# Kernel optimization log

Hardware: AMD Instinct MI355X
Metric: run time of the kernel (lower is better)

The kernel has to match this reference:

```python
import jax, jax.numpy as jnp
import numpy as np

B, L, D = 1, 2048, 1024
H = 16
HD = D // H
BETA = 0.08
EPS = 1e-6


def setup_inputs() -> dict:
    key = jax.random.key(0)
    ks = jax.random.split(key, 12)
    sc = 1.0 / np.sqrt(D)
    inp = {
        'x': jax.random.normal(ks[0], (B, L, D), dtype=jnp.float32),
        'Wq': jax.random.normal(ks[1], (D, D), dtype=jnp.float32) * sc,
        'bq': jnp.zeros((D,), jnp.float32),
        'Wk': jax.random.normal(ks[2], (D, D), dtype=jnp.float32) * sc,
        'bk': jnp.zeros((D,), jnp.float32),
        'Wv': jax.random.normal(ks[3], (D, D), dtype=jnp.float32) * sc,
        'bv': jnp.zeros((D,), jnp.float32),
        'Wo': jax.random.normal(ks[4], (D, D), dtype=jnp.float32) * sc,
        'bo': jnp.zeros((D,), jnp.float32),
        'Wp': jax.random.normal(ks[5], (2 * H, D), dtype=jnp.float32) * sc,
        'bp': jnp.zeros((2 * H,), jnp.float32),
        'gamma': jnp.full((H,), -2.197224577, jnp.float32),
    }
    return inp


def _split(t):  # [B,L,D] -> [B,H,L,hd]
    return t.reshape(B, L, H, HD).transpose(0, 2, 1, 3)


def reference(x, Wq, bq, Wk, bk, Wv, bv, Wo, bo, Wp, bp, gamma):
    q = _split(x @ Wq.T + bq)
    k = _split(x @ Wk.T + bk)
    v = _split(x @ Wv.T + bv)

    # phase features: [B,L,2H] -> [B,H,L,2], L2-normalized (torch F.normalize: x / max(||x||, eps))
    ph = (x @ Wp.T + bp).reshape(B, L, H, 2).transpose(0, 2, 1, 3)
    nrm = jnp.maximum(jnp.linalg.norm(ph, axis=-1, keepdims=True), EPS)
    ph = ph / nrm
    c, s = ph[..., 0], ph[..., 1]  # [B,H,L]

    # rank-2 Gram interference bias: cos(dphi) = c_i c_j + s_i s_j -> [B,H,L,L]
    inter = c[..., :, None] * c[..., None, :] + s[..., :, None] * s[..., None, :]
    head_gate = jax.nn.sigmoid(gamma) * BETA  # active_heads_mask all ones (fraction=1.0)
    bias = inter * head_gate[None, :, None, None]

    scores = jnp.einsum('bhqd,bhkd->bhqk', q, k) / jnp.sqrt(jnp.float32(HD)) + bias
    attn = jax.nn.softmax(scores, axis=-1)
    out = jnp.einsum('bhqk,bhkd->bhqd', attn, v)
    out = out.transpose(0, 2, 1, 3).reshape(B, L, D)
    return out @ Wo.T + bo
```

## Files before the change

### kernel.cpp

```cpp
#include <hip/hip_runtime.h>
#include <stdint.h>

typedef unsigned short u16;
typedef unsigned int u32;

#define L_SEQ 2048
#define DMODEL 1024
#define NHEAD 16

using f32x4 = __attribute__((ext_vector_type(4))) float;
using f32x16 = __attribute__((ext_vector_type(16))) float;
using s16x8 = __attribute__((ext_vector_type(8))) short;
using s16x4 = __attribute__((ext_vector_type(4))) short;

__device__ __forceinline__ u16 f2b(float f) {
    union { float f; uint32_t u; } v; v.f = f;
    uint32_t r = v.u + 0x7fffu + ((v.u >> 16) & 1u);
    return (u16)(r >> 16);
}

__device__ __forceinline__ float b2f(u16 x) {
    union { uint32_t u; float f; } v; v.u = ((uint32_t)x) << 16;
    return v.f;
}

__device__ __forceinline__ u32 pk2(float a, float b) {
    return (u32)f2b(a) | ((u32)f2b(b) << 16);
}

__device__ __forceinline__ u32 cvtpk(float lo, float hi_) {
    u32 r;
    asm("v_cvt_pk_bf16_f32 %0, %1, %2" : "=v"(r) : "v"(lo), "v"(hi_));
    return r;
}

__device__ __forceinline__ void gld16(const void* g, void* l) {
    __builtin_amdgcn_global_load_lds(
        (__attribute__((address_space(1))) void*)(uintptr_t)g,
        (__attribute__((address_space(3))) void*)(uintptr_t)l,
        16, 0, 0);
}

__global__ __launch_bounds__(256)
void k_conv(const float* __restrict__ x, const float* __restrict__ wq,
            const float* __restrict__ wk, const float* __restrict__ wv,
            const float* __restrict__ wo, const float* __restrict__ wp,
            const float* __restrict__ bp,
            u16* __restrict__ xb, u16* __restrict__ wqb, u16* __restrict__ wkb,
            u16* __restrict__ wvb, u16* __restrict__ wob, u16* __restrict__ wpb,
            float* __restrict__ bpPad) {
    const int NX = L_SEQ * DMODEL / 8;
    const int NW = DMODEL * DMODEL / 8;
    const int NCONV = (NX + 4 * NW) / 256;
    const int NP = 32 * DMODEL / 8;
    const int bid = blockIdx.x, tid = threadIdx.x;

    if (bid < NCONV) {
        int i = bid * 256 + tid;
        const float* src; u16* dst; int j;
        if (i < NX) { src = x; dst = xb; j = i; }
        else {
            int t = i - NX; int sel = t >> 17; j = t & (NW - 1);
            src = (sel == 0) ? wq : (sel == 1) ? wk : (sel == 2) ? wv : wo;
            dst = (sel == 0) ? wqb : (sel == 1) ? wkb : (sel == 2) ? wvb : wob;
        }
        const float4* s4 = (const float4*)src;
        float4 a = s4[2 * j], b = s4[2 * j + 1];
        union { s16x8 v; u16 u[8]; } o;
        o.u[0] = f2b(a.x); o.u[1] = f2b(a.y); o.u[2] = f2b(a.z); o.u[3] = f2b(a.w);
        o.u[4] = f2b(b.x); o.u[5] = f2b(b.y); o.u[6] = f2b(b.z); o.u[7] = f2b(b.w);
        ((s16x8*)dst)[j] = o.v;
        return;
    }
    if (bid < NCONV + 32) {
        int i2 = (bid - NCONV) * 256 + tid;
        union { s16x8 v; u16 u[8]; } o;
        if (i2 < NP) {
            const float4* s4 = (const float4*)wp;
            float4 a = s4[2 * i2], b = s4[2 * i2 + 1];
            o.u[0] = f2b(a.x); o.u[1] = f2b(a.y); o.u[2] = f2b(a.z); o.u[3] = f2b(a.w);
            o.u[4] = f2b(b.x); o.u[5] = f2b(b.y); o.u[6] = f2b(b.z); o.u[7] = f2b(b.w);
        } else {
#pragma unroll
            for (int j = 0; j < 8; ++j) o.u[j] = 0;
        }
        ((s16x8*)wpb)[i2] = o.v;
        return;
    }
    if (tid < 64) bpPad[tid] = (tid < 32) ? bp[tid] : 0.f;
}

template <int MODE>
__global__ __launch_bounds__(256, 2)
void k_gemm64(const u16* __restrict__ A,
              const u16* __restrict__ B0, const u16* __restrict__ B1, const u16* __restrict__ B2,
              const u16* __restrict__ B3,
              const float* __restrict__ c0, const float* __restrict__ c1, const float* __restrict__ c2,
              const float* __restrict__ c3,
              void* __restrict__ Out, u16* __restrict__ Vt, float* __restrict__ Ph,
              int ldo, int K) {
    __shared__ u16 As[128 * 64];
    __shared__ u16 Bs[64 * 64];
    const int tid = threadIdx.x;
    const int w = tid >> 6, lane = tid & 63;
    const int wr = w >> 1, wc = w & 1;
    const int u = lane & 15, g = lane >> 4;
    const int lr = lane >> 3;
    const int cb = lane & 7;
    const int mt = blockIdx.x, nt = blockIdx.y;
    const int seg = nt >> 4, ntl = nt & 15;
    const u16* Bp = (seg == 0) ? B0 : (seg == 1) ? B1 : (seg == 2) ? B2 : B3;
    const float* biasp = (seg == 0) ? c0 : (seg == 1) ? c1 : (seg == 2) ? c2 : c3;

    const u16* Ab = A + (size_t)(mt * 128 + w * 32) * K;
    const u16* Bb = Bp + (size_t)(ntl * 64) * K;
    char* asB = (char*)As;
    char* bsB = (char*)Bs;

    f32x4 acc[4][2] = {};

    for (int k0 = 0; k0 < K; k0 += 64) {
#pragma unroll
        for (int c = 0; c < 4; ++c)
            gld16(Ab + (size_t)(c * 8 + lr) * K + k0 + ((cb ^ lr) * 8),
                  asB + (w * 32 + c * 8) * 128);
#pragma unroll
        for (int t = 0; t < 2; ++t)
            gld16(Bb + (size_t)(t * 32 + w * 8 + lr) * K + k0 + ((cb ^ lr) * 8),
                  bsB + t * 4096 + w * 1024);
        __syncthreads();
        const int x0 = (g * 16) ^ ((u & 7) << 4);
#pragma unroll
        for (int ks = 0; ks < 2; ++ks) {
            s16x8 af[4], bf[2];
#pragma unroll
            for (int i = 0; i < 4; ++i)
                af[i] = *(const s16x8*)(asB + (wr * 64 + i * 16 + u) * 128 + (x0 ^ (ks * 64)));
#pragma unroll
            for (int j = 0; j < 2; ++j)
                bf[j] = *(const s16x8*)(bsB + (wc * 32 + j * 16 + u) * 128 + (x0 ^ (ks * 64)));
#pragma unroll
            for (int i = 0; i < 4; ++i)
#pragma unroll
                for (int j = 0; j < 2; ++j)
                    acc[i][j] = __builtin_amdgcn_mfma_f32_16x16x32_bf16(af[i], bf[j], acc[i][j], 0, 0, 0);
        }
        __syncthreads();
    }

#pragma unroll
    for (int i = 0; i < 4; ++i) {
#pragma unroll
        for (int j = 0; j < 2; ++j) {
            const int row0 = mt * 128 + wr * 64 + i * 16 + g * 4;
            const int col = nt * 64 + wc * 32 + j * 16 + u;
            const int colseg = ntl * 64 + wc * 32 + j * 16 + u;
            const float bias = biasp[colseg];
            if (MODE == 0 && seg == 2) {
                union { s16x4 v; u16 us[4]; } p;
#pragma unroll
                for (int r = 0; r < 4; ++r) p.us[r] = f2b(acc[i][j][r] + bias);
                *(s16x4*)(Vt + (size_t)colseg * L_SEQ + row0) = p.v;
            } else if (MODE == 0 && seg == 3) {
#pragma unroll
                for (int r = 0; r < 4; ++r)
                    Ph[(size_t)(row0 + r) * 64 + colseg] = acc[i][j][r] + bias;
            } else {
#pragma unroll
                for (int r = 0; r < 4; ++r) {
                    float val = acc[i][j][r] + bias;
                    if (MODE == 1)
                        ((float*)Out)[(size_t)(row0 + r) * ldo + col] = val;
                    else
                        ((u16*)Out)[(size_t)(row0 + r) * ldo + col] = f2b(val);
                }
            }
        }
    }
}

__global__ __launch_bounds__(256)
void k_norm(const float* __restrict__ ph, float2* __restrict__ CSph) {
    int t = blockIdx.x * 256 + threadIdx.x;
    int m = t >> 4, h = t & 15;
    float c = ph[(size_t)m * 64 + 2 * h];
    float s = ph[(size_t)m * 64 + 2 * h + 1];
    float inv = 1.0f / fmaxf(sqrtf(c * c + s * s), 1e-6f);
    CSph[(size_t)h * L_SEQ + m] = make_float2(c * inv, s * inv);
}

__global__ __launch_bounds__(256, 2)
void k_attn(const u16* __restrict__ QKV, const u16* __restrict__ VtG,
            const float2* __restrict__ CSph,
            const float* __restrict__ gamma,
            u16* __restrict__ Op0, u16* __restrict__ Op1, u16* __restrict__ Op2,
            float2* __restrict__ ML) {
    const int h = blockIdx.y;
    const int s = blockIdx.z;
    const int qb = blockIdx.x * 128;
    const int tid = threadIdx.x;
    const int ww = tid >> 6, lane = tid & 63;
    const int q5 = lane & 31, hi = lane >> 5;
    const int ld = 3 * DMODEL;
    const int NT = (s == 2) ? 10 : 11;
    const int kbase = s * 11 * 64;
    const int BUF = 64 * 64 * 2;
    const float MFIX = 8.0f;

    __shared__ u16 Ks[2][64 * 64];
    __shared__ u16 Vs[2][64 * 64];

    const float LOG2E = 1.44269504088896f;
    const float sig = 1.0f / (1.0f + __expf(-gamma[h]));
    const float gateA = 0.64f * sig;
    const float SC2 = 0.125f * LOG2E;

    const u16* Qp = QKV + h * 64;
    const u16* Kp = QKV + DMODEL + h * 64 + (size_t)kbase * ld;
    const u16* VtH = VtG + (size_t)h * 64 * L_SEQ + kbase;
    const float2* CS = CSph + (size_t)h * L_SEQ;

    const int qrow = qb + ww * 32 + q5;
    s16x8 bq[4];
#pragma unroll
    for (int d = 0; d < 4; ++d)
        bq[d] = *(const s16x8*)(Qp + (size_t)qrow * ld + d * 16 + hi * 8);
    s16x8 bcs;
    {
        float2 cs = CS[qrow];
        union { u32 w[4]; s16x8 v; } t = {};
        t.w[0] = hi ? 0u : pk2(cs.x, cs.y);
        bcs = t.v;
    }

    unsigned dstOff[2]; size_t srcK[2], srcV[2];
#pragma unroll
    for (int t = 0; t < 2; ++t) {
        int ci = (ww * 2 + t) * 64 + lane;
        int row = ci >> 3, cb = ci & 7;
        dstOff[t] = (unsigned)((ww * 2 + t) * 1024);
        srcK[t] = (size_t)row * ld + (size_t)((cb ^ (row & 7)) * 8);
        srcV[t] = (size_t)row * L_SEQ + (size_t)((cb ^ (row & 7)) * 8);
    }
    char* ksBase = (char*)Ks;
    char* vsBase = (char*)Vs;
    const int swz = (q5 & 7) << 4;

#pragma unroll
    for (int t = 0; t < 2; ++t) {
        gld16(Kp + srcK[t], ksBase + dstOff[t]);
        gld16(VtH + srcV[t], vsBase + dstOff[t]);
    }
    __syncthreads();

    float lsum = 0.f;
    f32x16 oA = {}, oB = {};

    for (int kt = 0; kt < NT; ++kt) {
        const int cur = kt & 1;
        const char* kCur = ksBase + cur * BUF;
        const char* vCur = vsBase + cur * BUF;

        if (kt + 1 < NT) {
            const u16* Kn = Kp + (size_t)(kt + 1) * 64 * ld;
            const u16* Vn = VtH + (size_t)(kt + 1) * 64;
            char* kN = ksBase + (cur ^ 1) * BUF;
            char* vN = vsBase + (cur ^ 1) * BUF;
#pragma unroll
            for (int t = 0; t < 2; ++t) {
                gld16(Kn + srcK[t], kN + dstOff[t]);
                gld16(Vn + srcV[t], vN + dstOff[t]);
            }
        }

        s16x8 acs0, acs1;
        {
            float2 c0 = CS[kbase + kt * 64 + q5];
            float2 c1 = CS[kbase + kt * 64 + 32 + q5];
            union { u32 w[4]; s16x8 v; } t0 = {}, t1 = {};
            t0.w[0] = hi ? 0u : pk2(gateA * c0.x, gateA * c0.y);
            t1.w[0] = hi ? 0u : pk2(gateA * c1.x, gateA * c1.y);
            acs0 = t0.v; acs1 = t1.v;
        }

        f32x16 sf0 = {}, sf1 = {};
        __builtin_amdgcn_s_setprio(1);
#pragma unroll
        for (int d = 0; d < 4; ++d) {
            s16x8 ak0 = *(const s16x8*)(kCur + q5 * 128 + ((d * 32 + hi * 16) ^ swz));
            s16x8 ak1 = *(const s16x8*)(kCur + (32 + q5) * 128 + ((d * 32 + hi * 16) ^ swz));
            sf0 = __builtin_amdgcn_mfma_f32_32x32x16_bf16(ak0, bq[d], sf0, 0, 0, 0);
            sf1 = __builtin_amdgcn_mfma_f32_32x32x16_bf16(ak1, bq[d], sf1, 0, 0, 0);
        }
        sf0 = __builtin_amdgcn_mfma_f32_32x32x16_bf16(acs0, bcs, sf0, 0, 0, 0);
        sf1 = __builtin_amdgcn_mfma_f32_32x32x16_bf16(acs1, bcs, sf1, 0, 0, 0);
        __builtin_amdgcn_s_setprio(0);

#pragma unroll
        for (int r = 0; r < 16; ++r) sf0[r] = __builtin_amdgcn_exp2f(__builtin_fmaf(sf0[r], SC2, -MFIX));
#pragma unroll
        for (int r = 0; r < 16; ++r) sf1[r] = __builtin_amdgcn_exp2f(__builtin_fmaf(sf1[r], SC2, -MFIX));

#pragma unroll
        for (int r = 0; r < 16; ++r) lsum += sf0[r] + sf1[r];

        __builtin_amdgcn_s_setprio(1);
#define PV_SUBTILE(SFV, HALF, SU)                                                              \
        {                                                                                      \
            u32 Aw  = cvtpk(SFV[(HALF) * 8 + 0], SFV[(HALF) * 8 + 1]);                         \
            u32 A2w = cvtpk(SFV[(HALF) * 8 + 2], SFV[(HALF) * 8 + 3]);                         \
            u32 Bw  = cvtpk(SFV[(HALF) * 8 + 4], SFV[(HALF) * 8 + 5]);                         \
            u32 B2w = cvtpk(SFV[(HALF) * 8 + 6], SFV[(HALF) * 8 + 7]);                         \
            u32 xw  = (u32)__shfl_xor((int)(hi ? Aw : Bw), 32);                                \
            u32 x2w = (u32)__shfl_xor((int)(hi ? A2w : B2w), 32);                              \
            union { u32 w[4]; s16x8 v; } pa;                                                   \
            pa.w[0] = hi ? xw : Aw;   pa.w[1] = hi ? x2w : A2w;                                \
            pa.w[2] = hi ? Bw : xw;   pa.w[3] = hi ? B2w : x2w;                                \
            s16x8 bvA = *(const s16x8*)(vCur + q5 * 128 + (((SU) * 32 + hi * 16) ^ swz));      \
            s16x8 bvB = *(const s16x8*)(vCur + (32 + q5) * 128 + (((SU) * 32 + hi * 16) ^ swz));\
            oA = __builtin_amdgcn_mfma_f32_32x32x16_bf16(pa.v, bvA, oA, 0, 0, 0);              \
            oB = __builtin_amdgcn_mfma_f32_32x32x16_bf16(pa.v, bvB, oB, 0, 0, 0);              \
        }
        PV_SUBTILE(sf0, 0, 0)
        PV_SUBTILE(sf0, 1, 1)
        PV_SUBTILE(sf1, 0, 2)
        PV_SUBTILE(sf1, 1, 3)
#undef PV_SUBTILE
        __builtin_amdgcn_s_setprio(0);

        __syncthreads();
    }

    lsum += __shfl_xor(lsum, 32);

    u16* OpS = (s == 0) ? Op0 : (s == 1) ? Op1 : Op2;
    float2* MLS = ML + (size_t)(s * NHEAD + h) * L_SEQ;
#pragma unroll
    for (int r = 0; r < 16; ++r) {
        int q_r = qb + ww * 32 + (r & 3) + 8 * (r >> 2) + 4 * hi;
        OpS[(size_t)q_r * DMODEL + h * 64 + q5] = f2b(oA[r]);
        OpS[(size_t)q_r * DMODEL + h * 64 + 32 + q5] = f2b(oB[r]);
    }
    if (hi == 0)
        MLS[qb + ww * 32 + q5] = make_float2(MFIX, lsum);
}

__global__ __launch_bounds__(256)
void k_comb(const u16* __restrict__ Op0, const u16* __restrict__ Op1,
            const u16* __restrict__ Op2, const float2* __restrict__ ML,
            u16* __restrict__ attnb) {
    int t = blockIdx.x * 256 + threadIdx.x;
    int row = t >> 7, cg = t & 127;
    int col0 = cg * 8, h = cg >> 3;
    float2 ml0 = ML[(size_t)h * L_SEQ + row];
    float2 ml1 = ML[(size_t)(NHEAD + h) * L_SEQ + row];
    float2 ml2 = ML[(size_t)(2 * NHEAD + h) * L_SEQ + row];
    float M = fmaxf(fmaxf(ml0.x, ml1.x), ml2.x);
    float a0 = __builtin_amdgcn_exp2f(ml0.x - M);
    float a1 = __builtin_amdgcn_exp2f(ml1.x - M);
    float a2 = __builtin_amdgcn_exp2f(ml2.x - M);
    float inv = 1.0f / (ml0.y * a0 + ml1.y * a1 + ml2.y * a2);
    a0 *= inv; a1 *= inv; a2 *= inv;
    union { s16x8 v; u16 us[8]; } o0, o1, o2, wout;
    size_t off = (size_t)row * DMODEL + col0;
    o0.v = *(const s16x8*)(Op0 + off);
    o1.v = *(const s16x8*)(Op1 + off);
    o2.v = *(const s16x8*)(Op2 + off);
#pragma unroll
    for (int j = 0; j < 8; ++j)
        wout.us[j] = f2b(b2f(o0.us[j]) * a0 + b2f(o1.us[j]) * a1 + b2f(o2.us[j]) * a2);
    *(s16x8*)(attnb + off) = wout.v;
}

extern "C" void kernel_launch(void* const* d_in, const int* in_sizes, int n_in,
                              void* d_out, int out_size, void* d_ws, size_t ws_size,
                              hipStream_t stream) {
    const float* x  = (const float*)d_in[0];
    const float* Wq = (const float*)d_in[1];
    const float* bq = (const float*)d_in[2];
    const float* Wk = (const float*)d_in[3];
    const float* bk = (const float*)d_in[4];
    const float* Wv = (const float*)d_in[5];
    const float* bv = (const float*)d_in[6];
    const float* Wo = (const float*)d_in[7];
    const float* bo = (const float*)d_in[8];
    const float* Wp = (const float*)d_in[9];
    const float* bp = (const float*)d_in[10];
    const float* gamma = (const float*)d_in[11];
    float* out = (float*)d_out;

    char* ws = (char*)d_ws;
    u16* xb = (u16*)ws;   ws += (size_t)L_SEQ * DMODEL * 2;
    u16* wqb = (u16*)ws;  ws += (size_t)DMODEL * DMODEL * 2;
    u16* wkb = (u16*)ws;  ws += (size_t)DMODEL * DMODEL * 2;
    u16* wvb = (u16*)ws;  ws += (size_t)DMODEL * DMODEL * 2;
    u16* wob = (u16*)ws;  ws += (size_t)DMODEL * DMODEL * 2;
    u16* qkv = (u16*)ws;  ws += (size_t)L_SEQ * 3 * DMODEL * 2;
    u16* attnb = (u16*)ws; ws += (size_t)L_SEQ * DMODEL * 2;
    u16* VtG = (u16*)ws;  ws += (size_t)DMODEL * L_SEQ * 2;
    float2* CSph = (float2*)ws; ws += (size_t)NHEAD * L_SEQ * 8;
    u16* wpb = (u16*)ws;  ws += (size_t)64 * DMODEL * 2;
    float* bpPad = (float*)ws; ws += 64 * 4;
    float* phtmp = (float*)ws; ws += (size_t)L_SEQ * 64 * 4;

    u16* Op0 = xb;
    u16* Op1 = wqb;
    u16* Op2 = attnb;
    float2* ML = (float2*)wvb;

    k_conv<<<3072 + 32 + 1, 256, 0, stream>>>(x, Wq, Wk, Wv, Wo, Wp, bp,
                                              xb, wqb, wkb, wvb, wob, wpb, bpPad);

    k_gemm64<0><<<dim3(16, 49), 256, 0, stream>>>(xb, wqb, wkb, wvb, wpb,
                                                  bq, bk, bv, bpPad,
                                                  (void*)qkv, VtG, phtmp, 3 * DMODEL, DMODEL);

    k_norm<<<L_SEQ * NHEAD / 256, 256, 0, stream>>>(phtmp, CSph);

    k_attn<<<dim3(L_SEQ / 128, NHEAD, 3), 256, 0, stream>>>(qkv, VtG, CSph, gamma,
                                                            Op0, Op1, Op2, ML);

    k_comb<<<L_SEQ * DMODEL / 8 / 256, 256, 0, stream>>>(Op0, Op1, Op2, ML, attnb);

    k_gemm64<1><<<dim3(16, 16), 256, 0, stream>>>(attnb, wob, wob, wob, wob,
                                                  bo, bo, bo, bo,
                                                  (void*)out, nullptr, nullptr, DMODEL, DMODEL);
}
```

Measured before the change: 85.38 us.

## Triple-buffer K/V tiles with vmcnt waits and preload phase terms into LDS

Moves the attention K/V staging from double to triple buffering. Two tiles are now in flight, and each iteration waits on a partial vmcnt count plus a raw s_barrier instead of a full __syncthreads. The gated cos/sin phase terms for all key tiles are also computed once into LDS up front, so the loop no longer does global loads and packing for them. This hides more global-load latency, at the cost of extra LDS (about 50 KB per block), which may reduce occupancy under launch_bounds(256,2), and of fragile hand-counted vmcnt values.

```diff
diff --git a/kernel.cpp b/kernel.cpp
--- a/kernel.cpp
+++ b/kernel.cpp
@@ -207,8 +207,9 @@
     const int BUF = 64 * 64 * 2;
     const float MFIX = 8.0f;
 
-    __shared__ u16 Ks[2][64 * 64];
-    __shared__ u16 Vs[2][64 * 64];
+    __shared__ u16 Ks[3][64 * 64];
+    __shared__ u16 Vs[3][64 * 64];
+    __shared__ u32 csLDS[11 * 32 * 2];
 
     const float LOG2E = 1.44269504088896f;
     const float sig = 1.0f / (1.0f + __expf(-gamma[h]));
@@ -247,39 +248,48 @@
     const int swz = (q5 & 7) << 4;
 
 #pragma unroll
-    for (int t = 0; t < 2; ++t) {
-        gld16(Kp + srcK[t], ksBase + dstOff[t]);
-        gld16(VtH + srcV[t], vsBase + dstOff[t]);
+    for (int pt = 0; pt < 3; ++pt) {
+        if (pt < NT) {
+            const u16* Kn = Kp + (size_t)pt * 64 * ld;
+            const u16* Vn = VtH + (size_t)pt * 64;
+#pragma unroll
+            for (int t = 0; t < 2; ++t) {
+                gld16(Kn + srcK[t], ksBase + pt * BUF + dstOff[t]);
+                gld16(Vn + srcV[t], vsBase + pt * BUF + dstOff[t]);
+            }
+        }
+    }
+    for (int t = tid; t < NT * 32; t += 256) {
+        int kt = t >> 5, qq = t & 31;
+        float2 c0 = CS[kbase + kt * 64 + qq];
+        float2 c1 = CS[kbase + kt * 64 + 32 + qq];
+        csLDS[t * 2] = pk2(gateA * c0.x, gateA * c0.y);
+        csLDS[t * 2 + 1] = pk2(gateA * c1.x, gateA * c1.y);
     }
     __syncthreads();
 
     float lsum = 0.f;
     f32x16 oA = {}, oB = {};
+    int cur = 0;
 
     for (int kt = 0; kt < NT; ++kt) {
-        const int cur = kt & 1;
         const char* kCur = ksBase + cur * BUF;
         const char* vCur = vsBase + cur * BUF;
 
-        if (kt + 1 < NT) {
-            const u16* Kn = Kp + (size_t)(kt + 1) * 64 * ld;
-            const u16* Vn = VtH + (size_t)(kt + 1) * 64;
-            char* kN = ksBase + (cur ^ 1) * BUF;
-            char* vN = vsBase + (cur ^ 1) * BUF;
-#pragma unroll
-            for (int t = 0; t < 2; ++t) {
-                gld16(Kn + srcK[t], kN + dstOff[t]);
-                gld16(Vn + srcV[t], vN + dstOff[t]);
-            }
-        }
+        if (kt + 2 < NT)      asm volatile("s_waitcnt vmcnt(8)" ::: "memory");
+        else if (kt + 1 < NT) asm volatile("s_waitcnt vmcnt(4)" ::: "memory");
+        else                  asm volatile("s_waitcnt vmcnt(0)" ::: "memory");
+        __builtin_amdgcn_sched_barrier(0);
+        __builtin_amdgcn_s_barrier();
+        __builtin_amdgcn_sched_barrier(0);
 
         s16x8 acs0, acs1;
         {
-            float2 c0 = CS[kbase + kt * 64 + q5];
-            float2 c1 = CS[kbase + kt * 64 + 32 + q5];
+            u32 w0 = csLDS[(kt * 32 + q5) * 2];
+            u32 w1 = csLDS[(kt * 32 + q5) * 2 + 1];
             union { u32 w[4]; s16x8 v; } t0 = {}, t1 = {};
-            t0.w[0] = hi ? 0u : pk2(gateA * c0.x, gateA * c0.y);
-            t1.w[0] = hi ? 0u : pk2(gateA * c1.x, gateA * c1.y);
+            t0.w[0] = hi ? 0u : w0;
+            t1.w[0] = hi ? 0u : w1;
             acs0 = t0.v; acs1 = t1.v;
         }
 
@@ -328,7 +338,20 @@
 #undef PV_SUBTILE
         __builtin_amdgcn_s_setprio(0);
 
-        __syncthreads();
+        __builtin_amdgcn_s_barrier();
+        __builtin_amdgcn_sched_barrier(0);
+        if (kt + 3 < NT) {
+            const u16* Kn = Kp + (size_t)(kt + 3) * 64 * ld;
+            const u16* Vn = VtH + (size_t)(kt + 3) * 64;
+            char* kN = ksBase + cur * BUF;
+            char* vN = vsBase + cur * BUF;
+#pragma unroll
+            for (int t = 0; t < 2; ++t) {
+                gld16(Kn + srcK[t], kN + dstOff[t]);
+                gld16(Vn + srcV[t], vN + dstOff[t]);
+            }
+        }
+        cur = (cur == 2) ? 0 : cur + 1;
     }
 
     lsum += __shfl_xor(lsum, 32);
```

After: 85.48 us. About the same (+0.1%).
